# Performance work log

Hardware: AMD Instinct MI355X
Metric: run time of the kernel (lower is better)

## Reference

```python
import jax, jax.numpy as jnp
import numpy as np

B, S, HID = 4, 4096, 1024
H, D = 16, 64  # num_head, attn_dim
EPS = 1e-6


def setup_inputs() -> dict:
    key = jax.random.key(0)
    ks = jax.random.split(key, 9)
    sc = 1.0 / np.sqrt(HID)
    return {
        "x": jax.random.normal(ks[0], (B, S, HID), jnp.float32),
        "Wq": jax.random.normal(ks[1], (HID, H * D), jnp.float32) * sc,
        "bq": jnp.zeros((H * D,), jnp.float32),
        "Wk": jax.random.normal(ks[2], (HID, H * D), jnp.float32) * sc,
        "bk": jnp.zeros((H * D,), jnp.float32),
        "Wv": jax.random.normal(ks[3], (HID, H * D), jnp.float32) * sc,
        "bv": jnp.zeros((H * D,), jnp.float32),
        "Wo": jax.random.normal(ks[4], (H * D, HID), jnp.float32) * sc,
        "bo": jnp.zeros((HID,), jnp.float32),
    }


def _phi(x):
    # feature_map == 'elu': elu(x) + 1
    return jax.nn.elu(x) + 1.0


def reference(x, Wq, bq, Wk, bk, Wv, bv, Wo, bo):
    bs, n, _ = x.shape
    # projections -> [b, n, h, d], then scan axis first -> [n, b, h, d]
    Q = _phi((x @ Wq + bq).reshape(bs, n, H, D)).transpose(1, 0, 2, 3)
    K = _phi((x @ Wk + bk).reshape(bs, n, H, D)).transpose(1, 0, 2, 3)
    V = (x @ Wv + bv).reshape(bs, n, H, D).transpose(1, 0, 2, 3)

    KV0 = jnp.zeros((bs, H, D, D), x.dtype)
    Ks0 = jnp.zeros((bs, H, D), x.dtype)

    def step(carry, qkv):
        KV, Ks = carry
        qi, ki, vi = qkv  # each [b, h, d]
        KV = KV + jnp.einsum('bhd,bhe->bhde', ki, vi)
        Ks = Ks + ki
        num = jnp.einsum('bhd,bhde->bhe', qi, KV)
        den = jnp.einsum('bhd,bhd->bh', qi, Ks)
        return (KV, Ks), num / (den[..., None] + EPS)

    _, out = jax.lax.scan(step, (KV0, Ks0), (Q, K, V))  # out: [n, b, h, d]
    out = out.transpose(1, 0, 2, 3).reshape(bs, n, H * D)
    return out @ Wo + bo
```

## Files before the change

### kernel.cpp

```cpp
#include <hip/hip_runtime.h>
#include <stdint.h>


#define DEVI __device__ __forceinline__

typedef __attribute__((ext_vector_type(8))) short bf16x8;
typedef __attribute__((ext_vector_type(4))) float f32x4;
typedef unsigned short u16;

DEVI u16 f2bf(float f) {
  union { float f; uint32_t u; } x; x.f = f;
  return (u16)((x.u + 0x7FFFu + ((x.u >> 16) & 1u)) >> 16);
}
DEVI float bf2f(u16 u) {
  union { uint32_t u; float f; } x; x.u = ((uint32_t)u) << 16;
  return x.f;
}
DEVI f32x4 mfma16(bf16x8 a, bf16x8 b, f32x4 c) {
  return __builtin_amdgcn_mfma_f32_16x16x32_bf16(a, b, c, 0, 0, 0);
}

typedef __attribute__((address_space(3))) void* lds_vp;
typedef const __attribute__((address_space(1))) void* glb_vp;
DEVI void gload_lds16(const void* g, void* l) {
  __builtin_amdgcn_global_load_lds((glb_vp)g, (lds_vp)l, 16, 0, 0);
}

static constexpr int Ss  = 4096;
static constexpr int Hh  = 16;
static constexpr int CC  = 64;
static constexpr int NCC = Ss / CC;

__global__ __launch_bounds__(256) void prep_k(const float* __restrict__ x,
                                              const float* __restrict__ w0,
                                              const float* __restrict__ w1,
                                              const float* __restrict__ w2,
                                              const float* __restrict__ w3,
                                              u16* __restrict__ xbf,
                                              u16* __restrict__ dqkv,
                                              u16* __restrict__ dwo) {
  __shared__ float tl[32][33];
  const int bid = blockIdx.x;
  if (bid < 8192) {
    const int i = bid * 256 + threadIdx.x;
    const float4* p = (const float4*)(x + (size_t)i * 8);
    const float4 a = p[0], b = p[1];
    union { uint4 v; u16 s[8]; } u;
    u.s[0] = f2bf(a.x); u.s[1] = f2bf(a.y); u.s[2] = f2bf(a.z); u.s[3] = f2bf(a.w);
    u.s[4] = f2bf(b.x); u.s[5] = f2bf(b.y); u.s[6] = f2bf(b.z); u.s[7] = f2bf(b.w);
    ((uint4*)xbf)[i] = u.v;
    return;
  }
  const int wz = bid - 8192;
  const int z = wz >> 10, wl = wz & 1023;
  const int bx = wl & 31, by = wl >> 5;
  const float* in = (z == 0) ? w0 : (z == 1) ? w1 : (z == 2) ? w2 : w3;
  u16* out = (z < 3) ? (dqkv + (size_t)z * 1024 * 1024) : dwo;
  const int tx = threadIdx.x & 31, ty = threadIdx.x >> 5;
#pragma unroll
  for (int j = 0; j < 4; ++j)
    tl[ty + j * 8][tx] = in[(size_t)(by * 32 + ty + j * 8) * 1024 + bx * 32 + tx];
  __syncthreads();
#pragma unroll
  for (int j = 0; j < 4; ++j)
    out[(size_t)(bx * 32 + ty + j * 8) * 1024 + by * 32 + tx] = f2bf(tl[tx][ty + j * 8]);
}

template <bool FUSED, bool OUTF32>
__global__ __launch_bounds__(512, 2) void gemm256_k(const u16* __restrict__ A,
                                                    const u16* __restrict__ BT,
                                                    const float* __restrict__ b0,
                                                    const float* __restrict__ b1,
                                                    const float* __restrict__ b2,
                                                    void* __restrict__ out,
                                                    int M, int K) {
  __shared__ __attribute__((aligned(16))) u16 lds[65536];
  const int t = threadIdx.x, lane = t & 63, w = t >> 6;
  const int wm = w >> 2, wn = w & 3;

  const int nx = gridDim.x;
  const int nwg = nx * gridDim.y;
  const int bid = blockIdx.y * nx + blockIdx.x;
  const int swz = (bid & 7) * (nwg >> 3) + (bid >> 3);
  const int bx = swz % nx, by = swz / nx;
  const int m0 = by * 256, n0 = bx * 256;

  const u16* gA = A + (size_t)m0 * K;
  const u16* gB = BT + (size_t)n0 * K;

  const int sr = t >> 2;
  const int sc = (t & 3) ^ ((sr >> 1) & 3);
  auto stage = [&](const u16* gm, u16* dst, int kof) {
    gload_lds16(gm + (size_t)sr * K + kof + sc * 8, dst + t * 8);
    gload_lds16(gm + (size_t)(sr + 128) * K + kof + sc * 8, dst + 4096 + t * 8);
  };

  f32x4 acc[8][4];
#pragma unroll
  for (int i = 0; i < 8; ++i)
#pragma unroll
    for (int j = 0; j < 4; ++j) acc[i][j] = f32x4{0.f, 0.f, 0.f, 0.f};

  stage(gA, lds, 0);          stage(gB, lds + 32768, 0);
  stage(gA, lds + 8192, 32);  stage(gB, lds + 40960, 32);

  const int fr = lane & 15, kq = lane >> 4;
  const int rdko = ((kq ^ ((fr >> 1) & 3)) << 3);
  const int arow0 = wm * 128 + fr;
  const int brow0 = wn * 64 + fr;

  const int nk = K >> 6;
  for (int kt = 0; kt < nk; ++kt) {
    const int buf = kt & 1;
    u16* Ax = lds + buf * 16384;
    u16* Bx = lds + 32768 + buf * 16384;
    u16* Ay = lds + (buf ^ 1) * 16384;
    u16* By = lds + 32768 + (buf ^ 1) * 16384;
    const bool pf = (kt + 1 < nk);
    const int kon = (kt + 1) << 6;
    bf16x8 af[8], bg0, bg1;

#pragma unroll
    for (int half = 0; half < 2; ++half) {
      u16* Axh = Ax + half * 8192;
      u16* Bxh = Bx + half * 8192;
      if (half == 0 || pf) asm volatile("s_waitcnt vmcnt(4)" ::: "memory");
      else                 asm volatile("s_waitcnt vmcnt(0)" ::: "memory");
      __builtin_amdgcn_s_barrier();
      if (pf) stage(gA, Ay + half * 8192, kon + half * 32);
#pragma unroll
      for (int fi = 0; fi < 8; ++fi)
        af[fi] = *(const bf16x8*)(Axh + (arow0 + fi * 16) * 32 + rdko);
      bg0 = *(const bf16x8*)(Bxh + brow0 * 32 + rdko);
      bg1 = *(const bf16x8*)(Bxh + (brow0 + 16) * 32 + rdko);
      asm volatile("s_waitcnt lgkmcnt(0)" ::: "memory");
      __builtin_amdgcn_sched_barrier(0);
      __builtin_amdgcn_s_setprio(1);
#pragma unroll
      for (int fi = 0; fi < 8; ++fi) {
        acc[fi][0] = mfma16(af[fi], bg0, acc[fi][0]);
        acc[fi][1] = mfma16(af[fi], bg1, acc[fi][1]);
      }
      __builtin_amdgcn_s_setprio(0);
      __builtin_amdgcn_sched_barrier(0);
      if (pf) stage(gB, By + half * 8192, kon + half * 32);
      bg0 = *(const bf16x8*)(Bxh + (brow0 + 32) * 32 + rdko);
      bg1 = *(const bf16x8*)(Bxh + (brow0 + 48) * 32 + rdko);
      asm volatile("s_waitcnt lgkmcnt(0)" ::: "memory");
      __builtin_amdgcn_sched_barrier(0);
      __builtin_amdgcn_s_setprio(1);
#pragma unroll
      for (int fi = 0; fi < 8; ++fi) {
        acc[fi][2] = mfma16(af[fi], bg0, acc[fi][2]);
        acc[fi][3] = mfma16(af[fi], bg1, acc[fi][3]);
      }
      __builtin_amdgcn_s_setprio(0);
      __builtin_amdgcn_sched_barrier(0);
    }
  }

  const int rowg = (lane >> 4) * 4;
  if constexpr (!OUTF32) {
    __syncthreads();
    const int seg  = FUSED ? (n0 >> 10) : 0;
    const int lcol0 = FUSED ? (n0 & 1023) : n0;
    const float* bp = b0;
    if constexpr (FUSED) bp = (seg == 0) ? b0 : (seg == 1) ? b1 : b2;
#pragma unroll
    for (int fj = 0; fj < 4; ++fj) {
      const int col = wn * 64 + fj * 16 + fr;
      const float bv = bp[lcol0 + col];
#pragma unroll
      for (int fi = 0; fi < 8; ++fi) {
#pragma unroll
        for (int rr = 0; rr < 4; ++rr) {
          const int row = wm * 128 + fi * 16 + rowg + rr;
          float v = acc[fi][fj][rr] + bv;
          if (FUSED && seg < 2) v = (v > 0.f) ? (v + 1.f) : __expf(v);
          lds[row * 256 + (((col >> 3) ^ ((row >> 2) & 31)) << 3) + (col & 7)] = f2bf(v);
        }
      }
    }
    __syncthreads();
    u16* outp = (u16*)out + (size_t)seg * M * 1024 + (size_t)m0 * 1024 + lcol0;
#pragma unroll
    for (int it = 0; it < 16; ++it) {
      const int g = it * 512 + t;
      const int row = g >> 5, c16 = g & 31;
      const uint4 v = *(const uint4*)&lds[row * 256 + ((c16 ^ ((row >> 2) & 31)) << 3)];
      *(uint4*)(outp + (size_t)row * 1024 + c16 * 8) = v;
    }
  } else {
    float* flds = (float*)lds;
#pragma unroll
    for (int pass = 0; pass < 2; ++pass) {
      __syncthreads();
      if (wm == pass) {
#pragma unroll
        for (int fj = 0; fj < 4; ++fj) {
          const int col = wn * 64 + fj * 16 + fr;
          const float bv = b0[n0 + col];
#pragma unroll
          for (int fi = 0; fi < 8; ++fi) {
#pragma unroll
            for (int rr = 0; rr < 4; ++rr) {
              const int rl = fi * 16 + rowg + rr;
              flds[rl * 256 + (((col >> 2) ^ ((rl >> 2) & 63)) << 2) + (col & 3)] =
                  acc[fi][fj][rr] + bv;
            }
          }
        }
      }
      __syncthreads();
      float* outp = (float*)out + (size_t)(m0 + pass * 128) * 1024 + n0;
#pragma unroll
      for (int it = 0; it < 16; ++it) {
        const int g = it * 512 + t;
        const int row = g >> 6, c16 = g & 63;
        const uint4 v = *(const uint4*)&flds[row * 256 + ((c16 ^ ((row >> 2) & 63)) << 2)];
        *(uint4*)(outp + (size_t)row * 1024 + n0 * 0 + c16 * 4) = v;
      }
    }
  }
}

__global__ __launch_bounds__(256) void chunk_kv_k(const u16* __restrict__ Kb,
                                                  const u16* __restrict__ Vb,
                                                  u16* __restrict__ KVTc,
                                                  float* __restrict__ Ksc) {
  const int c = blockIdx.x, h = blockIdx.y, b = blockIdx.z;
  __shared__ u16 KT[64][72], VT[64][72];
  const int t = threadIdx.x, lane = t & 63, w = t >> 6;
  {
    const int i = t >> 2, c0 = (t & 3) * 16;
    const size_t g = ((size_t)(b * Ss + c * CC + i)) * 1024 + h * 64 + c0;
    const u16* kp = Kb + g;
    const u16* vp = Vb + g;
#pragma unroll
    for (int j = 0; j < 16; ++j) { KT[c0 + j][i] = kp[j]; VT[c0 + j][i] = vp[j]; }
  }
  __syncthreads();
  f32x4 acc[4];
#pragma unroll
  for (int j = 0; j < 4; ++j) acc[j] = f32x4{0.f, 0.f, 0.f, 0.f};
  const int fr = lane & 15, kq = (lane >> 4) * 8;
#pragma unroll
  for (int kk = 0; kk < 2; ++kk) {
    const bf16x8 av = *(const bf16x8*)&VT[w * 16 + fr][kk * 32 + kq];
#pragma unroll
    for (int fj = 0; fj < 4; ++fj) {
      const bf16x8 bk = *(const bf16x8*)&KT[fj * 16 + fr][kk * 32 + kq];
      acc[fj] = mfma16(av, bk, acc[fj]);
    }
  }
  float ksv = 0.f;
  if (t < 64) {
#pragma unroll
    for (int ii = 0; ii < 8; ++ii) {
      const bf16x8 kv = *(const bf16x8*)&KT[t][ii * 8];
#pragma unroll
      for (int j = 0; j < 8; ++j) ksv += bf2f((u16)kv[j]);
    }
  }
  __syncthreads();
#pragma unroll
  for (int fj = 0; fj < 4; ++fj)
#pragma unroll
    for (int rr = 0; rr < 4; ++rr)
      VT[w * 16 + (lane >> 4) * 4 + rr][fj * 16 + fr] = f2bf(acc[fj][rr]);
  __syncthreads();
  const size_t base = ((size_t)((b * Hh + h) * NCC + c)) * 4096;
  {
    const int row = t >> 2, q8 = (t & 3) * 8;
    *(uint4*)(KVTc + base + (size_t)row * 64 + q8)      = *(const uint4*)&VT[row][q8];
    *(uint4*)(KVTc + base + (size_t)row * 64 + q8 + 32) = *(const uint4*)&VT[row][q8 + 32];
  }
  if (t < 64) Ksc[((size_t)((b * Hh + h) * NCC + c)) * 64 + t] = ksv;
}

__global__ __launch_bounds__(256) void prefix_k(const u16* __restrict__ KVTc,
                                                const float* __restrict__ Ksc,
                                                u16* __restrict__ KVpreT,
                                                float* __restrict__ Kspre) {
  const int bh = blockIdx.x, eg = blockIdx.y;
  const int t = threadIdx.x;
  const int e4 = eg * 1024 + t * 4;
  const u16* src = KVTc + (size_t)bh * NCC * 4096 + e4;
  u16* dst = KVpreT + (size_t)bh * NCC * 4096 + e4;
  const float* kss = Ksc + (size_t)bh * NCC * 64 + t;
  float* ksd = Kspre + (size_t)bh * NCC * 64 + t;
  const bool dok = (eg == 0 && t < 64);

  uint2 buf[8];
  float kbuf[8];
#pragma unroll
  for (int j = 0; j < 8; ++j) {
    buf[j] = *(const uint2*)(src + (size_t)j * 4096);
    kbuf[j] = dok ? kss[(size_t)j * 64] : 0.f;
  }
  float run[4] = {0.f, 0.f, 0.f, 0.f};
  float rk = 0.f;
  for (int g = 0; g < 8; ++g) {
#pragma unroll
    for (int j = 0; j < 8; ++j) {
      const int c = g * 8 + j;
      union { uint2 v; u16 s[4]; } in, ov;
      in.v = buf[j];
      const float kin = kbuf[j];
      if (c + 8 < NCC) {
        buf[j] = *(const uint2*)(src + (size_t)(c + 8) * 4096);
        if (dok) kbuf[j] = kss[(size_t)(c + 8) * 64];
      }
#pragma unroll
      for (int k = 0; k < 4; ++k) { ov.s[k] = f2bf(run[k]); run[k] += bf2f(in.s[k]); }
      *(uint2*)(dst + (size_t)c * 4096) = ov.v;
      if (dok) { ksd[(size_t)c * 64] = rk; rk += kin; }
    }
  }
}

__global__ __launch_bounds__(256) void chunk_out_k(const u16* __restrict__ Qb,
                                                   const u16* __restrict__ Kb,
                                                   const u16* __restrict__ Vb,
                                                   const u16* __restrict__ KVpreT,
                                                   const float* __restrict__ Kspre,
                                                   u16* __restrict__ attn) {
  const int c = blockIdx.x, h = blockIdx.y, b = blockIdx.z;
  const int bh = b * Hh + h;
  __shared__ u16 Ql[64][72], Kl[64][72], VT[64][72], Pl[64][72];
  __shared__ float den[64];
  const int t = threadIdx.x, lane = t & 63, w = t >> 6;

  {
    const int i = t >> 2, c0 = (t & 3) * 16;
    const size_t g = ((size_t)(b * Ss + c * CC + i)) * 1024 + h * 64 + c0;
    const uint4* qp = (const uint4*)(Qb + g);
    uint4* qd = (uint4*)&Ql[i][c0]; qd[0] = qp[0]; qd[1] = qp[1];
    const uint4* kp = (const uint4*)(Kb + g);
    uint4* kd = (uint4*)&Kl[i][c0]; kd[0] = kp[0]; kd[1] = kp[1];
    const u16* vp = Vb + g;
#pragma unroll
    for (int j = 0; j < 16; ++j) VT[c0 + j][i] = vp[j];
  }
  __syncthreads();

  f32x4 sacc[4];
#pragma unroll
  for (int fj = 0; fj < 4; ++fj) sacc[fj] = f32x4{0.f, 0.f, 0.f, 0.f};
#pragma unroll
  for (int kd = 0; kd < 2; ++kd) {
    const bf16x8 aq = *(const bf16x8*)&Ql[w * 16 + (lane & 15)][kd * 32 + (lane >> 4) * 8];
#pragma unroll
    for (int fj = 0; fj < 4; ++fj) {
      const bf16x8 bk = *(const bf16x8*)&Kl[fj * 16 + (lane & 15)][kd * 32 + (lane >> 4) * 8];
      sacc[fj] = mfma16(aq, bk, sacc[fj]);
    }
  }
  float rowsum[4] = {0.f, 0.f, 0.f, 0.f};
#pragma unroll
  for (int fj = 0; fj < 4; ++fj) {
#pragma unroll
    for (int rr = 0; rr < 4; ++rr) {
      const int i_loc = w * 16 + (lane >> 4) * 4 + rr;
      const int j_loc = fj * 16 + (lane & 15);
      const float v = (j_loc <= i_loc) ? sacc[fj][rr] : 0.f;
      Pl[i_loc][j_loc] = f2bf(v);
      rowsum[rr] += v;
    }
  }
#pragma unroll
  for (int off = 1; off < 16; off <<= 1) {
#pragma unroll
    for (int rr = 0; rr < 4; ++rr) rowsum[rr] += __shfl_xor(rowsum[rr], off, 64);
  }
  if ((lane & 15) == 0) {
#pragma unroll
    for (int rr = 0; rr < 4; ++rr) den[w * 16 + (lane >> 4) * 4 + rr] = rowsum[rr];
  }
  __syncthreads();
  {
    const int i = t >> 2, part = t & 3;
    const float* ksp = Kspre + ((size_t)(bh * NCC + c)) * 64 + part * 16;
    float s = 0.f;
#pragma unroll
    for (int sg = 0; sg < 2; ++sg) {
      const bf16x8 q = *(const bf16x8*)&Ql[i][part * 16 + sg * 8];
#pragma unroll
      for (int j = 0; j < 8; ++j) s += bf2f((u16)q[j]) * ksp[sg * 8 + j];
    }
    s += __shfl_xor(s, 1, 64);
    s += __shfl_xor(s, 2, 64);
    if (part == 0) den[i] = den[i] + s + 1e-6f;
  }
  __syncthreads();

  f32x4 oacc[4];
#pragma unroll
  for (int fj = 0; fj < 4; ++fj) oacc[fj] = f32x4{0.f, 0.f, 0.f, 0.f};
  const u16* kvb = KVpreT + ((size_t)(bh * NCC + c)) * 4096;
#pragma unroll
  for (int ks2 = 0; ks2 < 2; ++ks2) {
    const bf16x8 aq = *(const bf16x8*)&Ql[w * 16 + (lane & 15)][ks2 * 32 + (lane >> 4) * 8];
#pragma unroll
    for (int fj = 0; fj < 4; ++fj) {
      const bf16x8 bv =
          *(const bf16x8*)(kvb + (size_t)(fj * 16 + (lane & 15)) * 64 + ks2 * 32 + (lane >> 4) * 8);
      oacc[fj] = mfma16(aq, bv, oacc[fj]);
    }
  }
#pragma unroll
  for (int ks3 = 0; ks3 < 2; ++ks3) {
    const bf16x8 ap = *(const bf16x8*)&Pl[w * 16 + (lane & 15)][ks3 * 32 + (lane >> 4) * 8];
#pragma unroll
    for (int fj = 0; fj < 4; ++fj) {
      const bf16x8 bv = *(const bf16x8*)&VT[fj * 16 + (lane & 15)][ks3 * 32 + (lane >> 4) * 8];
      oacc[fj] = mfma16(ap, bv, oacc[fj]);
    }
  }
  __syncthreads();
#pragma unroll
  for (int fj = 0; fj < 4; ++fj) {
#pragma unroll
    for (int rr = 0; rr < 4; ++rr) {
      const int i_loc = w * 16 + (lane >> 4) * 4 + rr;
      Pl[i_loc][fj * 16 + (lane & 15)] = f2bf(oacc[fj][rr] / den[i_loc]);
    }
  }
  __syncthreads();
  {
    const int row = t >> 2, q8 = (t & 3) * 8;
    u16* ap2 = attn + ((size_t)(b * Ss + c * CC + row)) * 1024 + h * 64;
    *(uint4*)(ap2 + q8)      = *(const uint4*)&Pl[row][q8];
    *(uint4*)(ap2 + q8 + 32) = *(const uint4*)&Pl[row][q8 + 32];
  }
}

extern "C" void kernel_launch(void* const* d_in, const int* in_sizes, int n_in,
                              void* d_out, int out_size, void* d_ws, size_t ws_size,
                              hipStream_t stream) {
  (void)in_sizes; (void)n_in; (void)out_size; (void)ws_size;
  const float* x  = (const float*)d_in[0];
  const float* Wq = (const float*)d_in[1];
  const float* bq = (const float*)d_in[2];
  const float* Wk = (const float*)d_in[3];
  const float* bk = (const float*)d_in[4];
  const float* Wv = (const float*)d_in[5];
  const float* bv = (const float*)d_in[6];
  const float* Wo = (const float*)d_in[7];
  const float* bo = (const float*)d_in[8];
  float* out = (float*)d_out;
  char* ws = (char*)d_ws;

  size_t off = 0;
  auto take = [&](size_t bytes) { size_t r = off; off += (bytes + 255) & ~(size_t)255; return r; };
  const size_t WQKV_B = (size_t)3072 * 1024 * 2;
  const size_t WT_B   = (size_t)1024 * 1024 * 2;
  const size_t BIG_B  = (size_t)16384 * 1024 * 2;
  const size_t KVT_B  = (size_t)64 * NCC * 4096 * 2;
  const size_t KS_B   = (size_t)64 * NCC * 64 * 4;

  u16* WqkvT  = (u16*)(ws + take(WQKV_B));
  u16* WoT    = (u16*)(ws + take(WT_B));
  size_t shared_off = take(BIG_B);
  u16* xbf    = (u16*)(ws + shared_off);
  u16* KVTc   = (u16*)(ws + shared_off);
  u16* attn   = (u16*)(ws + shared_off);
  u16* Qb     = (u16*)(ws + take(BIG_B));
  u16* Kb     = (u16*)(ws + take(BIG_B));
  u16* Vb     = (u16*)(ws + take(BIG_B));
  u16* KVpreT = (u16*)(ws + take(KVT_B));
  float* Ksc  = (float*)(ws + take(KS_B));
  float* Kspre= (float*)(ws + take(KS_B));

  const dim3 blk(256);
  prep_k<<<dim3(12288), blk, 0, stream>>>(x, Wq, Wk, Wv, Wo, xbf, WqkvT, WoT);

  gemm256_k<true, false><<<dim3(12, 64), dim3(512), 0, stream>>>(
      xbf, WqkvT, bq, bk, bv, Qb, 16384, 1024);

  const dim3 gC(NCC, Hh, 4);
  chunk_kv_k<<<gC, blk, 0, stream>>>(Kb, Vb, KVTc, Ksc);
  prefix_k<<<dim3(64, 4), blk, 0, stream>>>(KVTc, Ksc, KVpreT, Kspre);
  chunk_out_k<<<gC, blk, 0, stream>>>(Qb, Kb, Vb, KVpreT, Kspre, attn);

  gemm256_k<false, true><<<dim3(4, 64), dim3(512), 0, stream>>>(
      attn, WoT, bo, NULL, NULL, out, 16384, 1024);
}
```

Baseline: 264.9 us.

## Shrink GEMM tile to 128x256 with single-stage K=32 double buffering

Replaces the 256x256 GEMM tile with a 128x256 tile, halving LDS use to 64KB and accumulator registers, and raises launch bounds to allow more resident blocks. The K loop now steps by 32 with a simple stage-next/wait/compute double buffer in place of the split-half interleaved prefetch schedule. The grid doubles in M for both the QKV and output projections. The aim is better occupancy and CU fill, particularly for the output GEMM, which previously had only 256 blocks. The cost is lower operand reuse per tile, more global traffic for B, and two barriers per shorter iteration.

Result: faster. 258.9 us, median of 2 (-2.3%).

```diff
diff --git a/kernel.cpp b/kernel.cpp
--- a/kernel.cpp
+++ b/kernel.cpp
@@ -67,14 +67,14 @@
 }
 
 template <bool FUSED, bool OUTF32>
-__global__ __launch_bounds__(512, 2) void gemm256_k(const u16* __restrict__ A,
+__global__ __launch_bounds__(512, 4) void gemm128_k(const u16* __restrict__ A,
                                                     const u16* __restrict__ BT,
                                                     const float* __restrict__ b0,
                                                     const float* __restrict__ b1,
                                                     const float* __restrict__ b2,
                                                     void* __restrict__ out,
                                                     int M, int K) {
-  __shared__ __attribute__((aligned(16))) u16 lds[65536];
+  __shared__ __attribute__((aligned(16))) u16 lds[32768];
   const int t = threadIdx.x, lane = t & 63, w = t >> 6;
   const int wm = w >> 2, wn = w & 3;
 
@@ -83,86 +83,73 @@
   const int bid = blockIdx.y * nx + blockIdx.x;
   const int swz = (bid & 7) * (nwg >> 3) + (bid >> 3);
   const int bx = swz % nx, by = swz / nx;
-  const int m0 = by * 256, n0 = bx * 256;
+  const int m0 = by * 128, n0 = bx * 256;
 
   const u16* gA = A + (size_t)m0 * K;
   const u16* gB = BT + (size_t)n0 * K;
 
   const int sr = t >> 2;
   const int sc = (t & 3) ^ ((sr >> 1) & 3);
-  auto stage = [&](const u16* gm, u16* dst, int kof) {
-    gload_lds16(gm + (size_t)sr * K + kof + sc * 8, dst + t * 8);
-    gload_lds16(gm + (size_t)(sr + 128) * K + kof + sc * 8, dst + 4096 + t * 8);
+  auto stage = [&](int kt2, int buf) {
+    const int kof = kt2 << 5;
+    gload_lds16(gA + (size_t)sr * K + kof + sc * 8, lds + buf * 4096 + t * 8);
+    gload_lds16(gB + (size_t)sr * K + kof + sc * 8, lds + 8192 + buf * 8192 + t * 8);
+    gload_lds16(gB + (size_t)(sr + 128) * K + kof + sc * 8,
+                lds + 8192 + buf * 8192 + 4096 + t * 8);
   };
 
-  f32x4 acc[8][4];
-#pragma unroll
-  for (int i = 0; i < 8; ++i)
+  f32x4 acc[4][4];
+#pragma unroll
+  for (int i = 0; i < 4; ++i)
 #pragma unroll
     for (int j = 0; j < 4; ++j) acc[i][j] = f32x4{0.f, 0.f, 0.f, 0.f};
 
-  stage(gA, lds, 0);          stage(gB, lds + 32768, 0);
-  stage(gA, lds + 8192, 32);  stage(gB, lds + 40960, 32);
+  stage(0, 0);
 
   const int fr = lane & 15, kq = lane >> 4;
-  const int rdko = ((kq ^ ((fr >> 1) & 3)) << 3);
-  const int arow0 = wm * 128 + fr;
+  const int arow0 = wm * 64 + fr;
   const int brow0 = wn * 64 + fr;
 
-  const int nk = K >> 6;
+  const int nk = K >> 5;
   for (int kt = 0; kt < nk; ++kt) {
     const int buf = kt & 1;
-    u16* Ax = lds + buf * 16384;
-    u16* Bx = lds + 32768 + buf * 16384;
-    u16* Ay = lds + (buf ^ 1) * 16384;
-    u16* By = lds + 32768 + (buf ^ 1) * 16384;
-    const bool pf = (kt + 1 < nk);
-    const int kon = (kt + 1) << 6;
-    bf16x8 af[8], bg0, bg1;
-
-#pragma unroll
-    for (int half = 0; half < 2; ++half) {
-      u16* Axh = Ax + half * 8192;
-      u16* Bxh = Bx + half * 8192;
-      if (half == 0 || pf) asm volatile("s_waitcnt vmcnt(4)" ::: "memory");
-      else                 asm volatile("s_waitcnt vmcnt(0)" ::: "memory");
-      __builtin_amdgcn_s_barrier();
-      if (pf) stage(gA, Ay + half * 8192, kon + half * 32);
-#pragma unroll
-      for (int fi = 0; fi < 8; ++fi)
-        af[fi] = *(const bf16x8*)(Axh + (arow0 + fi * 16) * 32 + rdko);
-      bg0 = *(const bf16x8*)(Bxh + brow0 * 32 + rdko);
-      bg1 = *(const bf16x8*)(Bxh + (brow0 + 16) * 32 + rdko);
-      asm volatile("s_waitcnt lgkmcnt(0)" ::: "memory");
-      __builtin_amdgcn_sched_barrier(0);
-      __builtin_amdgcn_s_setprio(1);
-#pragma unroll
-      for (int fi = 0; fi < 8; ++fi) {
-        acc[fi][0] = mfma16(af[fi], bg0, acc[fi][0]);
-        acc[fi][1] = mfma16(af[fi], bg1, acc[fi][1]);
-      }
-      __builtin_amdgcn_s_setprio(0);
-      __builtin_amdgcn_sched_barrier(0);
-      if (pf) stage(gB, By + half * 8192, kon + half * 32);
-      bg0 = *(const bf16x8*)(Bxh + (brow0 + 32) * 32 + rdko);
-      bg1 = *(const bf16x8*)(Bxh + (brow0 + 48) * 32 + rdko);
-      asm volatile("s_waitcnt lgkmcnt(0)" ::: "memory");
-      __builtin_amdgcn_sched_barrier(0);
-      __builtin_amdgcn_s_setprio(1);
-#pragma unroll
-      for (int fi = 0; fi < 8; ++fi) {
-        acc[fi][2] = mfma16(af[fi], bg0, acc[fi][2]);
-        acc[fi][3] = mfma16(af[fi], bg1, acc[fi][3]);
-      }
-      __builtin_amdgcn_s_setprio(0);
-      __builtin_amdgcn_sched_barrier(0);
-    }
+    if (kt + 1 < nk) {
+      stage(kt + 1, buf ^ 1);
+      asm volatile("s_waitcnt vmcnt(3)" ::: "memory");
+    } else {
+      asm volatile("s_waitcnt vmcnt(0)" ::: "memory");
+    }
+    __builtin_amdgcn_s_barrier();
+
+    const u16* Ab = lds + buf * 4096;
+    const u16* Bb = lds + 8192 + buf * 8192;
+    bf16x8 af[4], bg[4];
+#pragma unroll
+    for (int fi = 0; fi < 4; ++fi) {
+      const int row = arow0 + fi * 16;
+      af[fi] = *(const bf16x8*)(Ab + row * 32 + ((kq ^ ((row >> 1) & 3)) << 3));
+    }
+#pragma unroll
+    for (int fj = 0; fj < 4; ++fj) {
+      const int row = brow0 + fj * 16;
+      bg[fj] = *(const bf16x8*)(Bb + row * 32 + ((kq ^ ((row >> 1) & 3)) << 3));
+    }
+    asm volatile("s_waitcnt lgkmcnt(0)" ::: "memory");
+    __builtin_amdgcn_sched_barrier(0);
+    __builtin_amdgcn_s_setprio(1);
+#pragma unroll
+    for (int fi = 0; fi < 4; ++fi)
+#pragma unroll
+      for (int fj = 0; fj < 4; ++fj)
+        acc[fi][fj] = mfma16(af[fi], bg[fj], acc[fi][fj]);
+    __builtin_amdgcn_s_setprio(0);
+    __builtin_amdgcn_sched_barrier(0);
+    __builtin_amdgcn_s_barrier();
   }
 
   const int rowg = (lane >> 4) * 4;
   if constexpr (!OUTF32) {
-    __syncthreads();
-    const int seg  = FUSED ? (n0 >> 10) : 0;
+    const int seg   = FUSED ? (n0 >> 10) : 0;
     const int lcol0 = FUSED ? (n0 & 1023) : n0;
     const float* bp = b0;
     if constexpr (FUSED) bp = (seg == 0) ? b0 : (seg == 1) ? b1 : b2;
@@ -171,10 +158,10 @@
       const int col = wn * 64 + fj * 16 + fr;
       const float bv = bp[lcol0 + col];
 #pragma unroll
-      for (int fi = 0; fi < 8; ++fi) {
+      for (int fi = 0; fi < 4; ++fi) {
 #pragma unroll
         for (int rr = 0; rr < 4; ++rr) {
-          const int row = wm * 128 + fi * 16 + rowg + rr;
+          const int row = wm * 64 + fi * 16 + rowg + rr;
           float v = acc[fi][fj][rr] + bv;
           if (FUSED && seg < 2) v = (v > 0.f) ? (v + 1.f) : __expf(v);
           lds[row * 256 + (((col >> 3) ^ ((row >> 2) & 31)) << 3) + (col & 7)] = f2bf(v);
@@ -184,7 +171,7 @@
     __syncthreads();
     u16* outp = (u16*)out + (size_t)seg * M * 1024 + (size_t)m0 * 1024 + lcol0;
 #pragma unroll
-    for (int it = 0; it < 16; ++it) {
+    for (int it = 0; it < 8; ++it) {
       const int g = it * 512 + t;
       const int row = g >> 5, c16 = g & 31;
       const uint4 v = *(const uint4*)&lds[row * 256 + ((c16 ^ ((row >> 2) & 31)) << 3)];
@@ -201,7 +188,7 @@
           const int col = wn * 64 + fj * 16 + fr;
           const float bv = b0[n0 + col];
 #pragma unroll
-          for (int fi = 0; fi < 8; ++fi) {
+          for (int fi = 0; fi < 4; ++fi) {
 #pragma unroll
             for (int rr = 0; rr < 4; ++rr) {
               const int rl = fi * 16 + rowg + rr;
@@ -212,13 +199,12 @@
         }
       }
       __syncthreads();
-      float* outp = (float*)out + (size_t)(m0 + pass * 128) * 1024 + n0;
-#pragma unroll
-      for (int it = 0; it < 16; ++it) {
+#pragma unroll
+      for (int it = 0; it < 8; ++it) {
         const int g = it * 512 + t;
         const int row = g >> 6, c16 = g & 63;
         const uint4 v = *(const uint4*)&flds[row * 256 + ((c16 ^ ((row >> 2) & 63)) << 2)];
-        *(uint4*)(outp + (size_t)row * 1024 + n0 * 0 + c16 * 4) = v;
+        *(uint4*)((float*)out + (size_t)(m0 + pass * 64 + row) * 1024 + n0 + c16 * 4) = v;
       }
     }
   }
@@ -475,7 +461,7 @@
   const dim3 blk(256);
   prep_k<<<dim3(12288), blk, 0, stream>>>(x, Wq, Wk, Wv, Wo, xbf, WqkvT, WoT);
 
-  gemm256_k<true, false><<<dim3(12, 64), dim3(512), 0, stream>>>(
+  gemm128_k<true, false><<<dim3(12, 128), dim3(512), 0, stream>>>(
       xbf, WqkvT, bq, bk, bv, Qb, 16384, 1024);
 
   const dim3 gC(NCC, Hh, 4);
@@ -483,6 +469,6 @@
   prefix_k<<<dim3(64, 4), blk, 0, stream>>>(KVTc, Ksc, KVpreT, Kspre);
   chunk_out_k<<<gC, blk, 0, stream>>>(Qb, Kb, Vb, KVpreT, Kspre, attn);
 
-  gemm256_k<false, true><<<dim3(4, 64), dim3(512), 0, stream>>>(
+  gemm128_k<false, true><<<dim3(4, 128), dim3(512), 0, stream>>>(
       attn, WoT, bo, NULL, NULL, out, 16384, 1024);
 }
```
